# Performance work log

Measured on AMD Instinct MI355X. Metric: run time of the kernel, lower is better.

Reference implementation:

```python
import jax, jax.numpy as jnp
import numpy as np

N, E, G = 10000, 320000, 256
IN, H, FP, OUT = 128, 256, 5000, 138


def setup_inputs() -> dict:
    key = jax.random.key(0)
    ks = jax.random.split(key, 12)
    x = jax.random.normal(ks[0], (N, IN), dtype=jnp.float32)
    edge_index = jax.random.randint(ks[1], (2, E), 0, N, dtype=jnp.int64)
    batch_index = jnp.sort(jax.random.randint(ks[2], (N,), 0, G, dtype=jnp.int64))
    grover_fp = jax.random.normal(ks[3], (G, FP), dtype=jnp.float32)
    def lin(k, fan_in, fan_out):
        lim = 1.0 / np.sqrt(fan_in)
        return jax.random.uniform(k, (fan_in, fan_out), jnp.float32, -lim, lim)
    W1 = lin(ks[4], IN, H);            b1 = jnp.zeros((H,), jnp.float32)
    W2 = lin(ks[5], H, H);             b2 = jnp.zeros((H,), jnp.float32)
    Wm1 = lin(ks[6], H + FP, H);       bm1 = jnp.zeros((H,), jnp.float32)
    Wm2 = lin(ks[7], H, OUT);          bm2 = jnp.zeros((OUT,), jnp.float32)
    return {"x": x, "edge_index": edge_index, "batch_index": batch_index,
            "grover_fp": grover_fp, "W1": W1, "b1": b1, "W2": W2, "b2": b2,
            "Wm1": Wm1, "bm1": bm1, "Wm2": Wm2, "bm2": bm2}


def reference(x, edge_index, batch_index, grover_fp, W1, b1, W2, b2, Wm1, bm1, Wm2, bm2):
    n = x.shape[0]
    # GCNConv: add self-loops, symmetric degree normalization D^-1/2 (A+I) D^-1/2
    loop = jnp.arange(n, dtype=edge_index.dtype)
    src = jnp.concatenate([edge_index[0], loop])  # [E+N]
    dst = jnp.concatenate([edge_index[1], loop])
    deg = jax.ops.segment_sum(jnp.ones_like(src, dtype=x.dtype), dst, num_segments=n)
    dinv = jax.lax.rsqrt(jnp.maximum(deg, 1.0))
    norm = dinv[src] * dinv[dst]  # [E+N]

    def gcn(h, W, b):
        hw = h @ W                              # [N, H]
        msg = hw[src] * norm[:, None]           # gather + normalize
        return jax.ops.segment_sum(msg, dst, num_segments=n) + b  # scatter-add

    h = jax.nn.relu(gcn(x, W1, b1))
    h = jax.nn.relu(gcn(h, W2, b2))

    # global mean pool over graphs
    sums = jax.ops.segment_sum(h, batch_index, num_segments=G)        # [G, H]
    cnts = jax.ops.segment_sum(jnp.ones((n,), h.dtype), batch_index, num_segments=G)
    gnn_repr = sums / jnp.maximum(cnts, 1.0)[:, None]

    hcat = jnp.concatenate([gnn_repr, grover_fp], axis=-1)  # [G, H+FP]
    # MLP (dropout is identity in eval mode)
    return jax.nn.relu(hcat @ Wm1 + bm1) @ Wm2 + bm2        # [G, OUT]
```

## Files before the change

kernel.cpp:

```cpp
#include <hip/hip_runtime.h>

constexpr int N_NODES = 10000;
constexpr int E_EDGES = 320000;
constexpr int G_GRAPHS = 256;
constexpr int IN_F = 128;
constexpr int H_F = 256;
constexpr int FP_F = 5000;
constexpr int OUT_F = 138;
constexpr int KCAT = H_F + FP_F;
constexpr int KPAD = 5376;
constexpr int KZ = 21;
constexpr int DMAX = 128;

constexpr int ZB = (N_NODES + 255) / 256;
constexpr int W1TB = H_F * IN_F / 256;
constexpr int W2TB = H_F * H_F / 256;
constexpr int FPB = G_GRAPHS * (KPAD - H_F) / 8 / 256;
constexpr int HB = (E_EDGES + 255) / 256;
constexpr int WT_TILES = (KPAD / 64) * (H_F / 64);
constexpr int GB = 157 * 4;
constexpr int M1H = 160;
constexpr int AB = N_NODES / 4;

typedef __attribute__((ext_vector_type(8))) short short8;
typedef __attribute__((ext_vector_type(4))) float f32x4;

static __device__ __forceinline__ unsigned short f2bf(float f) {
    union { float f; unsigned u; } a; a.f = f;
    unsigned r = a.u + 0x7fffu + ((a.u >> 16) & 1u);
    return (unsigned short)(r >> 16);
}
static __device__ __forceinline__ float bf2f(unsigned short u) {
    union { unsigned u; float f; } a; a.u = ((unsigned)u) << 16;
    return a.f;
}

template <int K, bool AF32>
__device__ __forceinline__ void gemm_tile(unsigned short* a_lds, unsigned short* w_lds,
                                          const void* __restrict__ Asrc,
                                          const unsigned short* __restrict__ Wt,
                                          unsigned short* __restrict__ C,
                                          int bm0, int bn0, int tid) {
    constexpr int KB = 128;
    const int lane = tid & 63;
    const int wv = tid >> 6;

    f32x4 acc[4] = {};
    const int rA = wv * 16 + (lane & 15);
    const int kq = (lane >> 4) * 8;

    for (int kb = 0; kb < K; kb += KB) {
        for (int c = tid; c < 64 * KB / 8; c += 256) {
            int r = c >> 4;
            int k = (c & 15) * 8;
            int gr = bm0 + r;
            short8 v = {};
            if (gr < N_NODES) {
                if (AF32) {
                    const float* A = (const float*)Asrc;
                    const float* p = A + (size_t)gr * K + kb + k;
                    float4 lo = *reinterpret_cast<const float4*>(p);
                    float4 hi = *reinterpret_cast<const float4*>(p + 4);
                    v[0] = (short)f2bf(lo.x); v[1] = (short)f2bf(lo.y);
                    v[2] = (short)f2bf(lo.z); v[3] = (short)f2bf(lo.w);
                    v[4] = (short)f2bf(hi.x); v[5] = (short)f2bf(hi.y);
                    v[6] = (short)f2bf(hi.z); v[7] = (short)f2bf(hi.w);
                } else {
                    const unsigned short* A = (const unsigned short*)Asrc;
                    v = *reinterpret_cast<const short8*>(A + (size_t)gr * K + kb + k);
                }
            }
            int byte = r * (2 * KB) + ((2 * k) ^ ((r & 7) << 4));
            *reinterpret_cast<short8*>((char*)a_lds + byte) = v;
        }
        for (int c = tid; c < 64 * KB / 8; c += 256) {
            int r = c >> 4;
            int k = (c & 15) * 8;
            short8 v = *reinterpret_cast<const short8*>(Wt + (size_t)(bn0 + r) * K + kb + k);
            int byte = r * (2 * KB) + ((2 * k) ^ ((r & 7) << 4));
            *reinterpret_cast<short8*>((char*)w_lds + byte) = v;
        }
        __syncthreads();
#pragma unroll
        for (int t = 0; t < KB / 32; ++t) {
            const int k0 = t * 32 + kq;
            short8 af = *reinterpret_cast<const short8*>(
                (char*)a_lds + rA * (2 * KB) + ((2 * k0) ^ ((rA & 7) << 4)));
#pragma unroll
            for (int nt = 0; nt < 4; ++nt) {
                const int rW = nt * 16 + (lane & 15);
                short8 bfr = *reinterpret_cast<const short8*>(
                    (char*)w_lds + rW * (2 * KB) + ((2 * k0) ^ ((rW & 7) << 4)));
                acc[nt] = __builtin_amdgcn_mfma_f32_16x16x32_bf16(bfr, af, acc[nt], 0, 0, 0);
            }
        }
        __syncthreads();
    }

    const int row = bm0 + wv * 16 + (lane & 15);
    if (row < N_NODES) {
#pragma unroll
        for (int nt = 0; nt < 4; ++nt) {
            int col = bn0 + nt * 16 + (lane >> 4) * 4;
            ushort4 o;
            o.x = f2bf(acc[nt][0]);
            o.y = f2bf(acc[nt][1]);
            o.z = f2bf(acc[nt][2]);
            o.w = f2bf(acc[nt][3]);
            *reinterpret_cast<ushort4*>(C + (size_t)row * H_F + col) = o;
        }
    }
}

__device__ __forceinline__ void mlp1_tile(unsigned short* a_lds, unsigned short* w_lds,
                                          const unsigned short* __restrict__ hcat,
                                          const unsigned short* __restrict__ Wt,
                                          float* __restrict__ pz,
                                          int bm0, int bn0, int kz0, int tid) {
    constexpr int KB = 128;
    const int lane = tid & 63;
    const int wv = tid >> 6;

    f32x4 acc[4] = {};
    const int rA = wv * 16 + (lane & 15);
    const int kq = (lane >> 4) * 8;

    for (int kb = kz0; kb < kz0 + 256; kb += KB) {
        for (int c = tid; c < 64 * KB / 8; c += 256) {
            int r = c >> 4;
            int k = (c & 15) * 8;
            short8 v = *reinterpret_cast<const short8*>(hcat + (size_t)(bm0 + r) * KPAD + kb + k);
            int byte = r * (2 * KB) + ((2 * k) ^ ((r & 7) << 4));
            *reinterpret_cast<short8*>((char*)a_lds + byte) = v;
        }
        for (int c = tid; c < 64 * KB / 8; c += 256) {
            int r = c >> 4;
            int k = (c & 15) * 8;
            short8 v = *reinterpret_cast<const short8*>(Wt + (size_t)(bn0 + r) * KPAD + kb + k);
            int byte = r * (2 * KB) + ((2 * k) ^ ((r & 7) << 4));
            *reinterpret_cast<short8*>((char*)w_lds + byte) = v;
        }
        __syncthreads();
#pragma unroll
        for (int t = 0; t < KB / 32; ++t) {
            const int k0 = t * 32 + kq;
            short8 af = *reinterpret_cast<const short8*>(
                (char*)a_lds + rA * (2 * KB) + ((2 * k0) ^ ((rA & 7) << 4)));
#pragma unroll
            for (int nt = 0; nt < 4; ++nt) {
                const int rW = nt * 16 + (lane & 15);
                short8 bfr = *reinterpret_cast<const short8*>(
                    (char*)w_lds + rW * (2 * KB) + ((2 * k0) ^ ((rW & 7) << 4)));
                acc[nt] = __builtin_amdgcn_mfma_f32_16x16x32_bf16(bfr, af, acc[nt], 0, 0, 0);
            }
        }
        __syncthreads();
    }

    const int row = bm0 + wv * 16 + (lane & 15);
#pragma unroll
    for (int nt = 0; nt < 4; ++nt) {
        int col = bn0 + nt * 16 + (lane >> 4) * 4;
        float4 o; o.x = acc[nt][0]; o.y = acc[nt][1]; o.z = acc[nt][2]; o.w = acc[nt][3];
        *reinterpret_cast<float4*>(pz + (size_t)row * H_F + col) = o;
    }
}

__device__ __forceinline__ void agg_body(const unsigned short* __restrict__ hw,
                                         const int* __restrict__ cnt,
                                         const int* __restrict__ srcs_pad,
                                         const float* __restrict__ b,
                                         unsigned short* __restrict__ outp,
                                         int node_base, int tid) {
    const int lane = tid & 63;
    const int node = __builtin_amdgcn_readfirstlane(node_base + (tid >> 6));
    const float dd = rsqrtf((float)cnt[node] + 1.0f);
    const unsigned short* rowb = hw + lane * 4;
    const int* sp = srcs_pad + (node << 7);

    float a0, a1, a2, a3;
    {
        const ushort4 sv = *reinterpret_cast<const ushort4*>(hw + (size_t)node * H_F + lane * 4);
        const float4 bv = *reinterpret_cast<const float4*>(b + lane * 4);
        const float ddsq = dd * dd;
        a0 = bf2f(sv.x) * ddsq + bv.x;
        a1 = bf2f(sv.y) * ddsq + bv.y;
        a2 = bf2f(sv.z) * ddsq + bv.z;
        a3 = bf2f(sv.w) * ddsq + bv.w;
    }

    const int e1 = __builtin_amdgcn_readfirstlane(min(cnt[node], DMAX));
    int e = 0;
    for (; e + 8 <= e1; e += 8) {
        ushort4 v[8];
        float w[8];
#pragma unroll
        for (int q = 0; q < 8; ++q) {
            const int s = sp[e + q];
            w[q] = rsqrtf((float)cnt[s] + 1.0f) * dd;
            v[q] = *reinterpret_cast<const ushort4*>(rowb + (size_t)s * H_F);
        }
#pragma unroll
        for (int q = 0; q < 8; ++q) {
            a0 += bf2f(v[q].x) * w[q];
            a1 += bf2f(v[q].y) * w[q];
            a2 += bf2f(v[q].z) * w[q];
            a3 += bf2f(v[q].w) * w[q];
        }
    }
    for (; e < e1; ++e) {
        const int s = sp[e];
        const float w = rsqrtf((float)cnt[s] + 1.0f) * dd;
        const ushort4 v = *reinterpret_cast<const ushort4*>(rowb + (size_t)s * H_F);
        a0 += bf2f(v.x) * w;
        a1 += bf2f(v.y) * w;
        a2 += bf2f(v.z) * w;
        a3 += bf2f(v.w) * w;
    }
    ushort4 o;
    o.x = f2bf(fmaxf(a0, 0.0f));
    o.y = f2bf(fmaxf(a1, 0.0f));
    o.z = f2bf(fmaxf(a2, 0.0f));
    o.w = f2bf(fmaxf(a3, 0.0f));
    *reinterpret_cast<ushort4*>(outp + (size_t)node * H_F + lane * 4) = o;
}

__global__ void k_p1(const float* __restrict__ W1, const float* __restrict__ W2,
                     const float* __restrict__ gfp, int* __restrict__ cnt,
                     unsigned short* __restrict__ W1t, unsigned short* __restrict__ W2t,
                     unsigned short* __restrict__ hcat) {
    int w = blockIdx.x;
    if (w < ZB) {
        int i = w * 256 + threadIdx.x;
        if (i < N_NODES) cnt[i] = 0;
        return;
    }
    w -= ZB;
    if (w < W1TB) {
        int i = w * 256 + threadIdx.x;
        int c = i >> 7, k = i & 127;
        W1t[i] = f2bf(W1[(size_t)k * H_F + c]);
        return;
    }
    w -= W1TB;
    if (w < W2TB) {
        int i = w * 256 + threadIdx.x;
        int c = i >> 8, k = i & 255;
        W2t[i] = f2bf(W2[(size_t)k * H_F + c]);
        return;
    }
    w -= W2TB;
    {
        int idx = w * 256 + threadIdx.x;
        int g = idx / 640, k = (idx - g * 640) * 8;
        short8 v = {};
        if (k < FP_F) {
            const float* src = gfp + (size_t)g * FP_F + k;
            float4 lo = *reinterpret_cast<const float4*>(src);
            float4 hi = *reinterpret_cast<const float4*>(src + 4);
            v[0] = (short)f2bf(lo.x); v[1] = (short)f2bf(lo.y);
            v[2] = (short)f2bf(lo.z); v[3] = (short)f2bf(lo.w);
            v[4] = (short)f2bf(hi.x); v[5] = (short)f2bf(hi.y);
            v[6] = (short)f2bf(hi.z); v[7] = (short)f2bf(hi.w);
        }
        *reinterpret_cast<short8*>(hcat + (size_t)g * KPAD + H_F + k) = v;
    }
}

__global__ __launch_bounds__(256) void k_p2(const float* __restrict__ x,
                                            const unsigned short* __restrict__ W1t,
                                            unsigned short* __restrict__ Abf,
                                            const int* __restrict__ ei,
                                            int* __restrict__ cnt,
                                            int* __restrict__ srcs_pad,
                                            const float* __restrict__ Wm1,
                                            unsigned short* __restrict__ Wt) {
    __shared__ unsigned short a_lds[64 * 128];
    __shared__ unsigned short w_lds[64 * 128];
    int bx = blockIdx.x;
    if (bx < GB) {
        gemm_tile<IN_F, true>(a_lds, w_lds, x, W1t, Abf, (bx % 157) * 64, (bx / 157) * 64,
                              threadIdx.x);
        return;
    }
    bx -= GB;
    if (bx < HB) {
        int e = bx * 256 + threadIdx.x;
        if (e < E_EDGES) {
            int s = ei[e];
            int d = ei[E_EDGES + e];
            int p = atomicAdd(&cnt[d], 1);
            if (p < DMAX) srcs_pad[(d << 7) + p] = s;
        }
        return;
    }
    bx -= HB;
    float* tbuf = (float*)a_lds;
    const int k0 = (bx % (KPAD / 64)) * 64;
    const int c0 = (bx / (KPAD / 64)) * 64;
    for (int idx = threadIdx.x; idx < 64 * 64; idx += 256) {
        int r = idx >> 6, cc = idx & 63;
        int k = k0 + r;
        tbuf[r * 65 + cc] = (k < KCAT) ? Wm1[(size_t)k * H_F + c0 + cc] : 0.0f;
    }
    __syncthreads();
    for (int idx = threadIdx.x; idx < 64 * 64; idx += 256) {
        int r = idx >> 6, kk = idx & 63;
        Wt[(size_t)(c0 + r) * KPAD + k0 + kk] = f2bf(tbuf[kk * 65 + r]);
    }
}

__global__ __launch_bounds__(256) void k_p3(const unsigned short* __restrict__ Abf,
                                            const int* __restrict__ cnt,
                                            const int* __restrict__ srcs_pad,
                                            const float* __restrict__ b1,
                                            unsigned short* __restrict__ h1,
                                            const unsigned short* __restrict__ hcat,
                                            const unsigned short* __restrict__ Wm1t,
                                            float* __restrict__ partial) {
    __shared__ unsigned short a_lds[64 * 128];
    __shared__ unsigned short w_lds[64 * 128];
    int bx = blockIdx.x;
    if (bx < AB) {
        agg_body(Abf, cnt, srcs_pad, b1, h1, bx * 4, threadIdx.x);
        return;
    }
    bx -= AB;
    const int z = bx / 16 + 1;
    const int r = bx % 16;
    mlp1_tile(a_lds, w_lds, hcat, Wm1t, partial + (size_t)(z - 1) * (G_GRAPHS * H_F),
              (r & 3) * 64, (r >> 2) * 64, z * 256, threadIdx.x);
}

__global__ __launch_bounds__(256) void k_p4(const unsigned short* __restrict__ h1,
                                            const unsigned short* __restrict__ W2t,
                                            unsigned short* __restrict__ Abf) {
    __shared__ unsigned short a_lds[64 * 128];
    __shared__ unsigned short w_lds[64 * 128];
    gemm_tile<H_F, false>(a_lds, w_lds, h1, W2t, Abf, (blockIdx.x % 157) * 64,
                          (blockIdx.x / 157) * 64, threadIdx.x);
}

__global__ __launch_bounds__(256) void k_p5(const unsigned short* __restrict__ Abf,
                                            const int* __restrict__ cnt,
                                            const int* __restrict__ srcs_pad,
                                            const float* __restrict__ b2,
                                            unsigned short* __restrict__ h1,
                                            const unsigned short* __restrict__ hcat,
                                            const unsigned short* __restrict__ Wm1t,
                                            float* __restrict__ partial) {
    __shared__ unsigned short a_lds[64 * 128];
    __shared__ unsigned short w_lds[64 * 128];
    int bx = blockIdx.x;
    if (bx < AB) {
        agg_body(Abf, cnt, srcs_pad, b2, h1, bx * 4, threadIdx.x);
        return;
    }
    bx -= AB;
    const int z = bx / 16 + 11;
    const int r = bx % 16;
    mlp1_tile(a_lds, w_lds, hcat, Wm1t, partial + (size_t)(z - 1) * (G_GRAPHS * H_F),
              (r & 3) * 64, (r >> 2) * 64, z * 256, threadIdx.x);
}

__global__ void k_fin(const unsigned short* __restrict__ h1, const int* __restrict__ batch,
                      const unsigned short* __restrict__ Wm1t,
                      const float* __restrict__ partial, const float* __restrict__ bm1,
                      const float* __restrict__ Wm2, const float* __restrict__ bm2,
                      float* __restrict__ out) {
    __shared__ float m[H_F];
    __shared__ float hrow[H_F];
    const int g = blockIdx.x;
    const int j = threadIdx.x;
    int lo = 0, hi = N_NODES;
    while (lo < hi) { int mm = (lo + hi) >> 1; if (batch[mm] < g) lo = mm + 1; else hi = mm; }
    const int s = lo;
    lo = s; hi = N_NODES;
    while (lo < hi) { int mm = (lo + hi) >> 1; if (batch[mm] < g + 1) lo = mm + 1; else hi = mm; }
    const int e = lo;
    float c0 = 0.0f, c1 = 0.0f, c2 = 0.0f, c3 = 0.0f;
    int i = s;
    for (; i + 4 <= e; i += 4) {
        c0 += bf2f(h1[(size_t)(i + 0) * H_F + j]);
        c1 += bf2f(h1[(size_t)(i + 1) * H_F + j]);
        c2 += bf2f(h1[(size_t)(i + 2) * H_F + j]);
        c3 += bf2f(h1[(size_t)(i + 3) * H_F + j]);
    }
    for (; i < e; ++i) c0 += bf2f(h1[(size_t)i * H_F + j]);
    hrow[j] = ((c0 + c1) + (c2 + c3)) / fmaxf((float)(e - s), 1.0f);
    __syncthreads();

    float acc = bm1[j];
    for (int k = 0; k < H_F; k += 8) {
        short8 wv = *reinterpret_cast<const short8*>(Wm1t + (size_t)j * KPAD + k);
#pragma unroll
        for (int q = 0; q < 8; ++q) acc += hrow[k + q] * bf2f((unsigned short)wv[q]);
    }
    for (int z = 0; z < KZ - 1; ++z)
        acc += partial[((size_t)z * G_GRAPHS + g) * H_F + j];
    m[j] = fmaxf(acc, 0.0f);
    __syncthreads();
    if (j < OUT_F) {
        float a = bm2[j];
        for (int k = 0; k < H_F; ++k) a += m[k] * Wm2[k * OUT_F + j];
        out[g * OUT_F + j] = a;
    }
}

extern "C" void kernel_launch(void* const* d_in, const int* in_sizes, int n_in,
                              void* d_out, int out_size, void* d_ws, size_t ws_size,
                              hipStream_t stream) {
    const float* x       = (const float*)d_in[0];
    const int*   ei      = (const int*)d_in[1];
    const int*   batch   = (const int*)d_in[2];
    const float* gfp     = (const float*)d_in[3];
    const float* W1      = (const float*)d_in[4];
    const float* b1      = (const float*)d_in[5];
    const float* W2      = (const float*)d_in[6];
    const float* b2      = (const float*)d_in[7];
    const float* Wm1     = (const float*)d_in[8];
    const float* bm1     = (const float*)d_in[9];
    const float* Wm2     = (const float*)d_in[10];
    const float* bm2     = (const float*)d_in[11];
    float* out = (float*)d_out;

    unsigned short* W1t  = (unsigned short*)d_ws;
    unsigned short* W2t  = W1t + IN_F * H_F;
    unsigned short* Abf  = W2t + H_F * H_F;
    unsigned short* h1   = Abf + (size_t)N_NODES * H_F;
    unsigned short* hcat = h1 + (size_t)N_NODES * H_F;
    unsigned short* Wm1t = hcat + (size_t)G_GRAPHS * KPAD;
    float* partial = (float*)(Wm1t + (size_t)H_F * KPAD);
    int* cnt      = (int*)(partial + (size_t)(KZ - 1) * G_GRAPHS * H_F);
    int* srcs_pad = cnt + N_NODES;

    k_p1<<<ZB + W1TB + W2TB + FPB, 256, 0, stream>>>(W1, W2, gfp, cnt, W1t, W2t, hcat);

    k_p2<<<GB + HB + WT_TILES, 256, 0, stream>>>(x, W1t, Abf, ei, cnt, srcs_pad, Wm1, Wm1t);

    k_p3<<<AB + M1H, 256, 0, stream>>>(Abf, cnt, srcs_pad, b1, h1, hcat, Wm1t, partial);

    k_p4<<<GB, 256, 0, stream>>>(h1, W2t, Abf);

    k_p5<<<AB + M1H, 256, 0, stream>>>(Abf, cnt, srcs_pad, b2, h1, hcat, Wm1t, partial);

    k_fin<<<G_GRAPHS, H_F, 0, stream>>>(h1, batch, Wm1t, partial, bm1, Wm2, bm2, out);
}
```

Measured before the change: 117.8 us.

## Move MLP1 split-K tiles from aggregation kernels into the W2 GEMM kernel

The split-K MLP layer-1 tiles were co-launched with the two aggregation passes. They now all run together with the second-layer feature GEMM, and the aggregation passes become standalone kernels. The aim is to balance work per launch, so the gather-heavy aggregation no longer shares its grid and register budget with MFMA GEMM tiles, and to give the small GEMM kernel more blocks to fill the device. In exchange, the GEMM launch gets longer and the aggregation launches lose overlap with independent compute.

```diff
diff --git a/kernel.cpp b/kernel.cpp
--- a/kernel.cpp
+++ b/kernel.cpp
@@ -19,7 +19,7 @@
 constexpr int HB = (E_EDGES + 255) / 256;
 constexpr int WT_TILES = (KPAD / 64) * (H_F / 64);
 constexpr int GB = 157 * 4;
-constexpr int M1H = 160;
+constexpr int M1B = (KZ - 1) * 16;
 constexpr int AB = N_NODES / 4;
 
 typedef __attribute__((ext_vector_type(8))) short short8;
@@ -166,14 +166,13 @@
     }
 }
 
-__device__ __forceinline__ void agg_body(const unsigned short* __restrict__ hw,
-                                         const int* __restrict__ cnt,
-                                         const int* __restrict__ srcs_pad,
-                                         const float* __restrict__ b,
-                                         unsigned short* __restrict__ outp,
-                                         int node_base, int tid) {
-    const int lane = tid & 63;
-    const int node = __builtin_amdgcn_readfirstlane(node_base + (tid >> 6));
+__global__ __launch_bounds__(256) void k_agg(const unsigned short* __restrict__ hw,
+                                             const int* __restrict__ cnt,
+                                             const int* __restrict__ srcs_pad,
+                                             const float* __restrict__ b,
+                                             unsigned short* __restrict__ outp) {
+    const int lane = threadIdx.x & 63;
+    const int node = __builtin_amdgcn_readfirstlane(blockIdx.x * 4 + (threadIdx.x >> 6));
     const float dd = rsqrtf((float)cnt[node] + 1.0f);
     const unsigned short* rowb = hw + lane * 4;
     const int* sp = srcs_pad + (node << 7);
@@ -310,54 +309,22 @@
     }
 }
 
-__global__ __launch_bounds__(256) void k_p3(const unsigned short* __restrict__ Abf,
-                                            const int* __restrict__ cnt,
-                                            const int* __restrict__ srcs_pad,
-                                            const float* __restrict__ b1,
-                                            unsigned short* __restrict__ h1,
+__global__ __launch_bounds__(256) void k_p4(const unsigned short* __restrict__ h1,
+                                            const unsigned short* __restrict__ W2t,
+                                            unsigned short* __restrict__ Abf,
                                             const unsigned short* __restrict__ hcat,
                                             const unsigned short* __restrict__ Wm1t,
                                             float* __restrict__ partial) {
     __shared__ unsigned short a_lds[64 * 128];
     __shared__ unsigned short w_lds[64 * 128];
     int bx = blockIdx.x;
-    if (bx < AB) {
-        agg_body(Abf, cnt, srcs_pad, b1, h1, bx * 4, threadIdx.x);
-        return;
-    }
-    bx -= AB;
+    if (bx < GB) {
+        gemm_tile<H_F, false>(a_lds, w_lds, h1, W2t, Abf, (bx % 157) * 64, (bx / 157) * 64,
+                              threadIdx.x);
+        return;
+    }
+    bx -= GB;
     const int z = bx / 16 + 1;
-    const int r = bx % 16;
-    mlp1_tile(a_lds, w_lds, hcat, Wm1t, partial + (size_t)(z - 1) * (G_GRAPHS * H_F),
-              (r & 3) * 64, (r >> 2) * 64, z * 256, threadIdx.x);
-}
-
-__global__ __launch_bounds__(256) void k_p4(const unsigned short* __restrict__ h1,
-                                            const unsigned short* __restrict__ W2t,
-                                            unsigned short* __restrict__ Abf) {
-    __shared__ unsigned short a_lds[64 * 128];
-    __shared__ unsigned short w_lds[64 * 128];
-    gemm_tile<H_F, false>(a_lds, w_lds, h1, W2t, Abf, (blockIdx.x % 157) * 64,
-                          (blockIdx.x / 157) * 64, threadIdx.x);
-}
-
-__global__ __launch_bounds__(256) void k_p5(const unsigned short* __restrict__ Abf,
-                                            const int* __restrict__ cnt,
-                                            const int* __restrict__ srcs_pad,
-                                            const float* __restrict__ b2,
-                                            unsigned short* __restrict__ h1,
-                                            const unsigned short* __restrict__ hcat,
-                                            const unsigned short* __restrict__ Wm1t,
-                                            float* __restrict__ partial) {
-    __shared__ unsigned short a_lds[64 * 128];
-    __shared__ unsigned short w_lds[64 * 128];
-    int bx = blockIdx.x;
-    if (bx < AB) {
-        agg_body(Abf, cnt, srcs_pad, b2, h1, bx * 4, threadIdx.x);
-        return;
-    }
-    bx -= AB;
-    const int z = bx / 16 + 11;
     const int r = bx % 16;
     mlp1_tile(a_lds, w_lds, hcat, Wm1t, partial + (size_t)(z - 1) * (G_GRAPHS * H_F),
               (r & 3) * 64, (r >> 2) * 64, z * 256, threadIdx.x);
@@ -438,11 +405,11 @@
 
     k_p2<<<GB + HB + WT_TILES, 256, 0, stream>>>(x, W1t, Abf, ei, cnt, srcs_pad, Wm1, Wm1t);
 
-    k_p3<<<AB + M1H, 256, 0, stream>>>(Abf, cnt, srcs_pad, b1, h1, hcat, Wm1t, partial);
-
-    k_p4<<<GB, 256, 0, stream>>>(h1, W2t, Abf);
-
-    k_p5<<<AB + M1H, 256, 0, stream>>>(Abf, cnt, srcs_pad, b2, h1, hcat, Wm1t, partial);
+    k_agg<<<AB, 256, 0, stream>>>(Abf, cnt, srcs_pad, b1, h1);
+
+    k_p4<<<GB + M1B, 256, 0, stream>>>(h1, W2t, Abf, hcat, Wm1t, partial);
+
+    k_agg<<<AB, 256, 0, stream>>>(Abf, cnt, srcs_pad, b2, h1);
 
     k_fin<<<G_GRAPHS, H_F, 0, stream>>>(h1, batch, Wm1t, partial, bm1, Wm2, bm2, out);
 }
```

New measurement: 108.1 us. 8.2% less time.
